# Optimization experiments

Hardware: AMD Instinct MI355X
Metric: run time of the kernel (lower is better)

## Reference

```python
import jax, jax.numpy as jnp
import numpy as np

N, E, H, D = 100000, 800000, 4, 32
IN_DIM, OUT_DIM = 128, 128
NEG_SLOPE = 0.2


def setup_inputs() -> dict:
    key = jax.random.key(0)
    ks = jax.random.split(key, 10)
    x = jax.random.normal(ks[0], (N, IN_DIM), dtype=jnp.float32)
    edge_index = jax.random.randint(ks[1], (2, E), 0, N, dtype=jnp.int32)
    edge_type = jax.random.randint(ks[2], (E,), 0, 3, dtype=jnp.int32)
    s = 0.05  # xavier-ish small init scale
    Wq = jax.random.normal(ks[3], (IN_DIM, H * D), dtype=jnp.float32) * s
    Wk = jax.random.normal(ks[4], (IN_DIM, H * D), dtype=jnp.float32) * s
    Wv = jax.random.normal(ks[5], (IN_DIM, H * D), dtype=jnp.float32) * s
    attn_linear = jax.random.normal(ks[6], (1, H, 2 * D), dtype=jnp.float32) * s
    edge_embed_table = jax.random.normal(ks[7], (3, H * D), dtype=jnp.float32) * s
    Wo = jax.random.normal(ks[8], (H * D, OUT_DIM), dtype=jnp.float32) * s
    bo = jnp.zeros((OUT_DIM,), dtype=jnp.float32)
    return {"x": x, "edge_index": edge_index, "edge_type": edge_type,
            "Wq": Wq, "Wk": Wk, "Wv": Wv, "attn_linear": attn_linear,
            "edge_embed_table": edge_embed_table, "Wo": Wo, "bo": bo}


def reference(x, edge_index, edge_type, Wq, Wk, Wv, attn_linear, edge_embed_table, Wo, bo):
    src, dst = edge_index[0], edge_index[1]
    n = x.shape[0]
    q = (x @ Wq).reshape(n, H, D)
    k = (x @ Wk).reshape(n, H, D)
    v = (x @ Wv).reshape(n, H, D)
    attn_l = attn_linear[:, :, :D]   # (1,H,D)
    attn_r = attn_linear[:, :, D:]
    score_src = (q * attn_l).sum(-1)  # (N,H)
    score_dst = (k * attn_r).sum(-1)
    s = score_src[src] + score_dst[dst]            # (E,H)
    s = jnp.where(s >= 0, s, NEG_SLOPE * s)        # leaky_relu
    ee = edge_embed_table[edge_type].reshape(-1, H, D)  # (E,H,D)
    s = s + (q[src] * ee).sum(-1)
    # sparse softmax over edges grouped by dst (detached max, clamped at -100)
    max_s = jnp.full((n, H), -jnp.inf, dtype=s.dtype).at[dst].max(jax.lax.stop_gradient(s))
    max_s = jnp.maximum(max_s, -100.0)
    exp_s = jnp.exp(s - max_s[dst])
    sum_exp = jax.ops.segment_sum(exp_s, dst, num_segments=n)
    a = jnp.minimum(exp_s / (sum_exp[dst] + 1e-6), 1.0)  # (E,H)
    msgs = a[:, :, None] * v[src]                        # (E,H,D)
    out = jax.ops.segment_sum(msgs, dst, num_segments=n) # (N,H,D)
    out = jnp.clip(out, -50.0, 50.0).reshape(n, H * D)
    return out @ Wo + bo
```

## Files before the change

kernel.cpp:

```cpp
#include <hip/hip_runtime.h>
#include <cstdint>

#define HEADS 4
#define DD    32
#define HD    128
#define SCOL  32
#define NEGS  0.2f

typedef __attribute__((ext_vector_type(8))) short bf16x8;
typedef __attribute__((ext_vector_type(4))) float f32x4;

__device__ __forceinline__ float bl(unsigned u) { return __uint_as_float(u << 16); }
__device__ __forceinline__ float bh(unsigned u) { return __uint_as_float(u & 0xffff0000u); }
__device__ __forceinline__ unsigned short f2b(float f) {
    unsigned u = __float_as_uint(f);
    u += 0x7fffu + ((u >> 16) & 1u);
    return (unsigned short)(u >> 16);
}

__global__ void k_buildC(const float* __restrict__ Wq, const float* __restrict__ Wk,
                         const float* __restrict__ attn, const float* __restrict__ ee,
                         float* __restrict__ C) {
    int tid = blockIdx.x*blockDim.x + threadIdx.x;
    if (tid >= HD*SCOL) return;
    int i = tid >> 5, c = tid & 31;
    float s = 0.f;
    if (c < 8) {
        int h = c & 3;
        const float* w = ((c < 4) ? Wq : Wk) + i*HD + h*DD;
        const float* a = attn + h*64 + ((c < 4) ? 0 : DD);
        #pragma unroll
        for (int d = 0; d < DD; ++d) s += w[d]*a[d];
    } else if (c < 20) {
        int idx = c - 8; int ty = idx >> 2; int h = idx & 3;
        const float* w  = Wq + i*HD + h*DD;
        const float* em = ee + ty*HD + h*DD;
        #pragma unroll
        for (int d = 0; d < DD; ++d) s += w[d]*em[d];
    }
    C[i*SCOL + c] = s;
}

__global__ void k_pack(const float* __restrict__ Wv, const float* __restrict__ C,
                       const float* __restrict__ Wo,
                       unsigned short* __restrict__ Bpv, unsigned short* __restrict__ Bpo) {
    int id = blockIdx.x*256 + threadIdx.x;
    if (id < 20480) {
        int j = id & 7, l = (id >> 3) & 63, tk = id >> 9;
        int t = tk >> 2, kk = tk & 3;
        int k = kk*32 + (l >> 4)*8 + j;
        int n = t*16 + (l & 15);
        float val = (n < HD) ? Wv[k*HD + n] : C[k*SCOL + (n - HD)];
        Bpv[id] = f2b(val);
    } else if (id < 36864) {
        int o = id - 20480;
        int j = o & 7, l = (o >> 3) & 63, tk = o >> 9;
        int t = tk >> 2, kk = tk & 3;
        int k = kk*32 + (l >> 4)*8 + j;
        int n = t*16 + (l & 15);
        Bpo[o] = f2b(Wo[k*HD + n]);
    }
}

__global__ __launch_bounds__(256)
void k_vproj(const float* __restrict__ x, const unsigned short* __restrict__ Bpv,
             unsigned short* __restrict__ vbf, float* __restrict__ scores, int N) {
    __shared__ unsigned short xs[64*136];
    const int t = threadIdx.x;
    const int nbase = blockIdx.x * 64;
    const float4* xg = (const float4*)x;
    #pragma unroll
    for (int k = 0; k < 8; ++k) {
        int fi = t + k*256;
        int row = fi >> 5, c4 = fi & 31;
        int node = nbase + row;
        float4 val = make_float4(0.f,0.f,0.f,0.f);
        if (node < N) val = xg[(size_t)nbase*32 + fi];
        unsigned short p[4] = { f2b(val.x), f2b(val.y), f2b(val.z), f2b(val.w) };
        *(uint2*)((char*)xs + row*272 + c4*8) = *(const uint2*)p;
    }
    __syncthreads();
    const int wid = t >> 6, l = t & 63;
    const int lr = l & 15, lg = l >> 4;
    bf16x8 a[4];
    #pragma unroll
    for (int kk = 0; kk < 4; ++kk)
        a[kk] = *(const bf16x8*)((const char*)xs + (16*wid + lr)*272 + kk*64 + lg*16);
    const bf16x8* Bp = (const bf16x8*)Bpv;
    #pragma unroll
    for (int ct = 0; ct < 10; ++ct) {
        f32x4 acc = {0.f, 0.f, 0.f, 0.f};
        #pragma unroll
        for (int kk = 0; kk < 4; ++kk)
            acc = __builtin_amdgcn_mfma_f32_16x16x32_bf16(a[kk], Bp[(ct*4 + kk)*64 + l], acc, 0, 0, 0);
        if (ct < 8) {
            int col = ct*16 + lr;
            #pragma unroll
            for (int r = 0; r < 4; ++r) {
                int node = nbase + 16*wid + lg*4 + r;
                if (node < N) vbf[(size_t)node*HD + col] = f2b(acc[r]);
            }
        } else {
            int col = (ct - 8)*16 + lr;
            #pragma unroll
            for (int r = 0; r < 4; ++r) {
                int node = nbase + 16*wid + lg*4 + r;
                if (node < N) scores[(size_t)node*SCOL + col] = acc[r];
            }
        }
    }
}

__global__ void k_count(const int* __restrict__ ei, int* __restrict__ counts, int E) {
    int e = blockIdx.x*256 + threadIdx.x;
    if (e < E) atomicAdd(&counts[ei[E + e]], 1);
}

__global__ __launch_bounds__(256)
void k_scan1(const int* __restrict__ counts, int* __restrict__ off,
             int* __restrict__ bsum, int N) {
    __shared__ int sh[256];
    int t = threadIdx.x;
    int base = blockIdx.x*2048 + t*8;
    int vals[8]; int s = 0;
    #pragma unroll
    for (int k = 0; k < 8; ++k) {
        int idx = base + k;
        int cv = (idx < N) ? counts[idx] : 0;
        s += cv; vals[k] = s;
    }
    sh[t] = s;
    __syncthreads();
    for (int o = 1; o < 256; o <<= 1) {
        int v2 = (t >= o) ? sh[t-o] : 0;
        __syncthreads();
        sh[t] += v2;
        __syncthreads();
    }
    int excl = (t > 0) ? sh[t-1] : 0;
    #pragma unroll
    for (int k = 0; k < 8; ++k) {
        int idx = base + k;
        if (idx < N) off[idx+1] = excl + vals[k];
    }
    if (t == 255) bsum[blockIdx.x] = sh[255];
    if (blockIdx.x == 0 && t == 0) off[0] = 0;
}
__global__ void k_scan2(int* __restrict__ bsum, int nb) {
    __shared__ int sh[256];
    int t = threadIdx.x;
    sh[t] = (t < nb) ? bsum[t] : 0;
    __syncthreads();
    for (int o = 1; o < 256; o <<= 1) {
        int v2 = (t >= o) ? sh[t-o] : 0;
        __syncthreads();
        sh[t] += v2;
        __syncthreads();
    }
    if (t < nb) bsum[t] = (t > 0) ? sh[t-1] : 0;
}
__global__ void k_scan3(int* __restrict__ off, const int* __restrict__ bsum, int N) {
    int i = blockIdx.x*256 + threadIdx.x;
    if (i < N) off[i+1] += bsum[i >> 11];
}

__global__ void k_fill(const int* __restrict__ ei, const int* __restrict__ et,
                       const float* __restrict__ scores, int* __restrict__ off,
                       int* __restrict__ ssrc, float4* __restrict__ sw4, int E) {
    int e = blockIdx.x*256 + threadIdx.x;
    if (e >= E) return;
    int src = ei[e], dst = ei[E + e], ty = et[e];
    const float* ps = scores + (size_t)src*SCOL;
    const float* pd = scores + (size_t)dst*SCOL;
    float4 a = *(const float4*)(ps);
    float4 b = *(const float4*)(pd + 4);
    float4 q = *(const float4*)(ps + 8 + 4*ty);
    float4 w;
    float t0;
    t0 = a.x + b.x; w.x = __expf(((t0 >= 0.f) ? t0 : NEGS*t0) + q.x);
    t0 = a.y + b.y; w.y = __expf(((t0 >= 0.f) ? t0 : NEGS*t0) + q.y);
    t0 = a.z + b.z; w.z = __expf(((t0 >= 0.f) ? t0 : NEGS*t0) + q.z);
    t0 = a.w + b.w; w.w = __expf(((t0 >= 0.f) ? t0 : NEGS*t0) + q.w);
    int slot = atomicAdd(&off[dst], 1);
    ssrc[slot] = src;
    sw4[slot]  = w;
}

__global__ __launch_bounds__(256)
void k_agg(const int* __restrict__ off, const int* __restrict__ ssrc,
           const float4* __restrict__ sw4, const unsigned short* __restrict__ vbf,
           unsigned short* __restrict__ outbf, int N) {
    const int wid  = threadIdx.x >> 6;
    const int lane = threadIdx.x & 63;
    const int n = blockIdx.x*4 + wid;
    if (n >= N) return;
    const int start = (n > 0) ? off[n-1] : 0;
    const int end   = off[n];
    const int g  = lane >> 4;
    const int dl = lane & 15;
    const int hh = dl >> 2;
    const float* wf = (const float*)sw4;
    float z = 0.f;
    float c0=0.f,c1=0.f,c2=0.f,c3=0.f,c4=0.f,c5=0.f,c6=0.f,c7=0.f;
    int  sl0 = start + g, sl1 = sl0 + 4;
    bool p0 = sl0 < end, p1 = sl1 < end;
    float w0 = 0.f, w1 = 0.f;
    uint4 v0 = make_uint4(0,0,0,0), v1 = make_uint4(0,0,0,0);
    if (p0) { int s = ssrc[sl0]; w0 = wf[(size_t)sl0*4 + hh];
              v0 = *(const uint4*)&vbf[(size_t)s*HD + dl*8]; }
    if (p1) { int s = ssrc[sl1]; w1 = wf[(size_t)sl1*4 + hh];
              v1 = *(const uint4*)&vbf[(size_t)s*HD + dl*8]; }
    while (p0) {
        int  sl2 = sl0 + 8;
        bool p2 = sl2 < end;
        float w2 = 0.f; uint4 v2 = make_uint4(0,0,0,0);
        if (p2) { int s = ssrc[sl2]; w2 = wf[(size_t)sl2*4 + hh];
                  v2 = *(const uint4*)&vbf[(size_t)s*HD + dl*8]; }
        z  += w0;
        c0 += w0*bl(v0.x); c1 += w0*bh(v0.x);
        c2 += w0*bl(v0.y); c3 += w0*bh(v0.y);
        c4 += w0*bl(v0.z); c5 += w0*bh(v0.z);
        c6 += w0*bl(v0.w); c7 += w0*bh(v0.w);
        sl0 = sl1; p0 = p1; w0 = w1; v0 = v1;
        sl1 = sl2; p1 = p2; w1 = w2; v1 = v2;
    }
    #pragma unroll
    for (int o = 16; o <= 32; o <<= 1) {
        z  += __shfl_xor(z, o);
        c0 += __shfl_xor(c0, o); c1 += __shfl_xor(c1, o);
        c2 += __shfl_xor(c2, o); c3 += __shfl_xor(c3, o);
        c4 += __shfl_xor(c4, o); c5 += __shfl_xor(c5, o);
        c6 += __shfl_xor(c6, o); c7 += __shfl_xor(c7, o);
    }
    if (g == 0) {
        float r = 1.f/(z + 1e-6f);
        unsigned short p[8] = { f2b(c0*r), f2b(c1*r), f2b(c2*r), f2b(c3*r),
                                f2b(c4*r), f2b(c5*r), f2b(c6*r), f2b(c7*r) };
        *(uint4*)&outbf[(size_t)n*HD + dl*8] = *(const uint4*)p;
    }
}

__global__ __launch_bounds__(256)
void k_out(const unsigned short* __restrict__ accbf, const unsigned short* __restrict__ Bpo,
           const float* __restrict__ bo, float* __restrict__ out, int N) {
    const int t = threadIdx.x;
    const int wid = t >> 6, l = t & 63;
    const int tile = blockIdx.x*4 + wid;
    if (tile*16 >= N) return;
    const int lr = l & 15, lg = l >> 4;
    const int r0 = tile*16;
    bf16x8 a[4];
    #pragma unroll
    for (int kk = 0; kk < 4; ++kk)
        a[kk] = *(const bf16x8*)&accbf[(size_t)(r0 + lr)*HD + kk*32 + lg*8];
    const bf16x8* Bp = (const bf16x8*)Bpo;
    #pragma unroll
    for (int ct = 0; ct < 8; ++ct) {
        f32x4 acc = {0.f, 0.f, 0.f, 0.f};
        #pragma unroll
        for (int kk = 0; kk < 4; ++kk)
            acc = __builtin_amdgcn_mfma_f32_16x16x32_bf16(a[kk], Bp[(ct*4 + kk)*64 + l], acc, 0, 0, 0);
        int col = ct*16 + lr;
        float bias = bo[col];
        #pragma unroll
        for (int r = 0; r < 4; ++r) {
            int node = r0 + lg*4 + r;
            if (node < N) out[(size_t)node*HD + col] = acc[r] + bias;
        }
    }
}

extern "C" void kernel_launch(void* const* d_in, const int* in_sizes, int n_in,
                              void* d_out, int out_size, void* d_ws, size_t ws_size,
                              hipStream_t stream) {
    const float* x    = (const float*)d_in[0];
    const int*   ei   = (const int*)  d_in[1];
    const int*   et   = (const int*)  d_in[2];
    const float* Wq   = (const float*)d_in[3];
    const float* Wk   = (const float*)d_in[4];
    const float* Wv   = (const float*)d_in[5];
    const float* attn = (const float*)d_in[6];
    const float* ee   = (const float*)d_in[7];
    const float* Wo   = (const float*)d_in[8];
    const float* bo   = (const float*)d_in[9];
    float* out = (float*)d_out;
    const int N = in_sizes[0] / HD;
    const int E = in_sizes[2];

    char* w = (char*)d_ws;
    auto alloc = [&](size_t bytes) -> void* {
        void* p = (void*)w;
        w += (bytes + 255) & ~(size_t)255;
        return p;
    };
    float*          C      = (float*)         alloc((size_t)HD*SCOL*sizeof(float));
    unsigned short* Bpv    = (unsigned short*)alloc((size_t)20480*sizeof(unsigned short));
    unsigned short* Bpo    = (unsigned short*)alloc((size_t)16384*sizeof(unsigned short));
    unsigned short* vbf    = (unsigned short*)alloc((size_t)N*HD*sizeof(unsigned short));
    float*          scores = (float*)         alloc((size_t)N*SCOL*sizeof(float));
    int*            counts = (int*)           alloc((size_t)N*sizeof(int));
    int*            off    = (int*)           alloc((size_t)(N+1)*sizeof(int));
    int*            bsum   = (int*)           alloc(4096);
    int*            ssrc   = (int*)           alloc((size_t)E*sizeof(int));
    float4*         sw4    = (float4*)        alloc((size_t)E*sizeof(float4));
    unsigned short* outbf  = (unsigned short*)alloc((size_t)N*HD*sizeof(unsigned short));

    hipMemsetAsync(counts, 0, (size_t)N*sizeof(int), stream);
    k_buildC<<<(HD*SCOL + 255)/256, 256, 0, stream>>>(Wq, Wk, attn, ee, C);
    k_pack<<<144, 256, 0, stream>>>(Wv, C, Wo, Bpv, Bpo);
    k_vproj<<<(N + 63)/64, 256, 0, stream>>>(x, Bpv, vbf, scores, N);
    k_count<<<(E + 255)/256, 256, 0, stream>>>(ei, counts, E);
    const int nb = (N + 2047)/2048;
    k_scan1<<<nb, 256, 0, stream>>>(counts, off, bsum, N);
    k_scan2<<<1, 256, 0, stream>>>(bsum, nb);
    k_scan3<<<(N + 255)/256, 256, 0, stream>>>(off, bsum, N);
    k_fill<<<(E + 255)/256, 256, 0, stream>>>(ei, et, scores, off, ssrc, sw4, E);
    k_agg<<<(N + 3)/4, 256, 0, stream>>>(off, ssrc, sw4, vbf, outbf, N);
    k_out<<<(N + 63)/64, 256, 0, stream>>>(outbf, Bpo, bo, out, N);
}
```

Before: 192.2 us.

## Move edge-weight computation into aggregation and pack src/type into one word

The fill kernel no longer computes and stores per-edge float4 exp weights. It only scatters a packed 32-bit (src | type<<20) entry per edge. The aggregation kernel now gathers the source scores and computes the leaky-relu/exp weight itself, which removes the 16-byte weight write and re-read per edge. Each lane now covers 16 features (8 edges in flight per wave instead of 4), so more accumulators are live and register pressure rises. It also adds extra gathers of scores rows and relies on src fitting in 20 bits.

```diff
diff --git a/kernel.cpp b/kernel.cpp
--- a/kernel.cpp
+++ b/kernel.cpp
@@ -164,31 +164,18 @@
     if (i < N) off[i+1] += bsum[i >> 11];
 }
 
-__global__ void k_fill(const int* __restrict__ ei, const int* __restrict__ et,
-                       const float* __restrict__ scores, int* __restrict__ off,
-                       int* __restrict__ ssrc, float4* __restrict__ sw4, int E) {
+__global__ void k_slot(const int* __restrict__ ei, const int* __restrict__ et,
+                       int* __restrict__ off, unsigned* __restrict__ pk, int E) {
     int e = blockIdx.x*256 + threadIdx.x;
     if (e >= E) return;
     int src = ei[e], dst = ei[E + e], ty = et[e];
-    const float* ps = scores + (size_t)src*SCOL;
-    const float* pd = scores + (size_t)dst*SCOL;
-    float4 a = *(const float4*)(ps);
-    float4 b = *(const float4*)(pd + 4);
-    float4 q = *(const float4*)(ps + 8 + 4*ty);
-    float4 w;
-    float t0;
-    t0 = a.x + b.x; w.x = __expf(((t0 >= 0.f) ? t0 : NEGS*t0) + q.x);
-    t0 = a.y + b.y; w.y = __expf(((t0 >= 0.f) ? t0 : NEGS*t0) + q.y);
-    t0 = a.z + b.z; w.z = __expf(((t0 >= 0.f) ? t0 : NEGS*t0) + q.z);
-    t0 = a.w + b.w; w.w = __expf(((t0 >= 0.f) ? t0 : NEGS*t0) + q.w);
     int slot = atomicAdd(&off[dst], 1);
-    ssrc[slot] = src;
-    sw4[slot]  = w;
+    pk[slot] = (unsigned)src | ((unsigned)ty << 20);
 }
 
 __global__ __launch_bounds__(256)
-void k_agg(const int* __restrict__ off, const int* __restrict__ ssrc,
-           const float4* __restrict__ sw4, const unsigned short* __restrict__ vbf,
+void k_agg(const int* __restrict__ off, const unsigned* __restrict__ pk,
+           const float* __restrict__ scores, const unsigned short* __restrict__ vbf,
            unsigned short* __restrict__ outbf, int N) {
     const int wid  = threadIdx.x >> 6;
     const int lane = threadIdx.x & 63;
@@ -196,47 +183,67 @@
     if (n >= N) return;
     const int start = (n > 0) ? off[n-1] : 0;
     const int end   = off[n];
-    const int g  = lane >> 4;
-    const int dl = lane & 15;
-    const int hh = dl >> 2;
-    const float* wf = (const float*)sw4;
+    const int g  = lane >> 3;
+    const int dl = lane & 7;
+    const int hh = dl >> 1;
+    const float sd = scores[(size_t)n*SCOL + 4 + hh];
     float z = 0.f;
-    float c0=0.f,c1=0.f,c2=0.f,c3=0.f,c4=0.f,c5=0.f,c6=0.f,c7=0.f;
-    int  sl0 = start + g, sl1 = sl0 + 4;
-    bool p0 = sl0 < end, p1 = sl1 < end;
-    float w0 = 0.f, w1 = 0.f;
-    uint4 v0 = make_uint4(0,0,0,0), v1 = make_uint4(0,0,0,0);
-    if (p0) { int s = ssrc[sl0]; w0 = wf[(size_t)sl0*4 + hh];
-              v0 = *(const uint4*)&vbf[(size_t)s*HD + dl*8]; }
-    if (p1) { int s = ssrc[sl1]; w1 = wf[(size_t)sl1*4 + hh];
-              v1 = *(const uint4*)&vbf[(size_t)s*HD + dl*8]; }
+    float c[16];
+    #pragma unroll
+    for (int i = 0; i < 16; ++i) c[i] = 0.f;
+
+    int  sl0 = start + g;
+    bool p0 = sl0 < end;
+    float f0 = 0.f, q0 = 0.f;
+    uint4 va0 = make_uint4(0,0,0,0), vb0 = make_uint4(0,0,0,0);
+    if (p0) {
+        unsigned pe = pk[sl0];
+        int s = pe & 0xFFFFF, ty = pe >> 20;
+        const float* ps = scores + (size_t)s*SCOL;
+        f0 = ps[hh]; q0 = ps[8 + 4*ty + hh];
+        const unsigned short* pv = vbf + (size_t)s*HD + dl*16;
+        va0 = *(const uint4*)pv; vb0 = *(const uint4*)(pv + 8);
+    }
     while (p0) {
-        int  sl2 = sl0 + 8;
-        bool p2 = sl2 < end;
-        float w2 = 0.f; uint4 v2 = make_uint4(0,0,0,0);
-        if (p2) { int s = ssrc[sl2]; w2 = wf[(size_t)sl2*4 + hh];
-                  v2 = *(const uint4*)&vbf[(size_t)s*HD + dl*8]; }
-        z  += w0;
-        c0 += w0*bl(v0.x); c1 += w0*bh(v0.x);
-        c2 += w0*bl(v0.y); c3 += w0*bh(v0.y);
-        c4 += w0*bl(v0.z); c5 += w0*bh(v0.z);
-        c6 += w0*bl(v0.w); c7 += w0*bh(v0.w);
-        sl0 = sl1; p0 = p1; w0 = w1; v0 = v1;
-        sl1 = sl2; p1 = p2; w1 = w2; v1 = v2;
-    }
-    #pragma unroll
-    for (int o = 16; o <= 32; o <<= 1) {
-        z  += __shfl_xor(z, o);
-        c0 += __shfl_xor(c0, o); c1 += __shfl_xor(c1, o);
-        c2 += __shfl_xor(c2, o); c3 += __shfl_xor(c3, o);
-        c4 += __shfl_xor(c4, o); c5 += __shfl_xor(c5, o);
-        c6 += __shfl_xor(c6, o); c7 += __shfl_xor(c7, o);
+        int  sl1 = sl0 + 8;
+        bool p1 = sl1 < end;
+        float f1 = 0.f, q1 = 0.f;
+        uint4 va1 = make_uint4(0,0,0,0), vb1 = make_uint4(0,0,0,0);
+        if (p1) {
+            unsigned pe = pk[sl1];
+            int s = pe & 0xFFFFF, ty = pe >> 20;
+            const float* ps = scores + (size_t)s*SCOL;
+            f1 = ps[hh]; q1 = ps[8 + 4*ty + hh];
+            const unsigned short* pv = vbf + (size_t)s*HD + dl*16;
+            va1 = *(const uint4*)pv; vb1 = *(const uint4*)(pv + 8);
+        }
+        float t = f0 + sd;
+        float w = __expf(((t >= 0.f) ? t : NEGS*t) + q0);
+        z += w;
+        c[0] += w*bl(va0.x); c[1] += w*bh(va0.x);
+        c[2] += w*bl(va0.y); c[3] += w*bh(va0.y);
+        c[4] += w*bl(va0.z); c[5] += w*bh(va0.z);
+        c[6] += w*bl(va0.w); c[7] += w*bh(va0.w);
+        c[8] += w*bl(vb0.x); c[9] += w*bh(vb0.x);
+        c[10]+= w*bl(vb0.y); c[11]+= w*bh(vb0.y);
+        c[12]+= w*bl(vb0.z); c[13]+= w*bh(vb0.z);
+        c[14]+= w*bl(vb0.w); c[15]+= w*bh(vb0.w);
+        sl0 = sl1; p0 = p1; f0 = f1; q0 = q1; va0 = va1; vb0 = vb1;
+    }
+    #pragma unroll
+    for (int o = 8; o <= 32; o <<= 1) {
+        z += __shfl_xor(z, o);
+        #pragma unroll
+        for (int i = 0; i < 16; ++i) c[i] += __shfl_xor(c[i], o);
     }
     if (g == 0) {
         float r = 1.f/(z + 1e-6f);
-        unsigned short p[8] = { f2b(c0*r), f2b(c1*r), f2b(c2*r), f2b(c3*r),
-                                f2b(c4*r), f2b(c5*r), f2b(c6*r), f2b(c7*r) };
-        *(uint4*)&outbf[(size_t)n*HD + dl*8] = *(const uint4*)p;
+        unsigned short pbuf[16];
+        #pragma unroll
+        for (int i = 0; i < 16; ++i) pbuf[i] = f2b(c[i]*r);
+        unsigned short* po = outbf + (size_t)n*HD + dl*16;
+        *(uint4*)po       = *(const uint4*)pbuf;
+        *(uint4*)(po + 8) = *(const uint4*)(pbuf + 8);
     }
 }
 
@@ -301,8 +308,7 @@
     int*            counts = (int*)           alloc((size_t)N*sizeof(int));
     int*            off    = (int*)           alloc((size_t)(N+1)*sizeof(int));
     int*            bsum   = (int*)           alloc(4096);
-    int*            ssrc   = (int*)           alloc((size_t)E*sizeof(int));
-    float4*         sw4    = (float4*)        alloc((size_t)E*sizeof(float4));
+    unsigned*       pk     = (unsigned*)      alloc((size_t)E*sizeof(unsigned));
     unsigned short* outbf  = (unsigned short*)alloc((size_t)N*HD*sizeof(unsigned short));
 
     hipMemsetAsync(counts, 0, (size_t)N*sizeof(int), stream);
@@ -314,7 +320,7 @@
     k_scan1<<<nb, 256, 0, stream>>>(counts, off, bsum, N);
     k_scan2<<<1, 256, 0, stream>>>(bsum, nb);
     k_scan3<<<(N + 255)/256, 256, 0, stream>>>(off, bsum, N);
-    k_fill<<<(E + 255)/256, 256, 0, stream>>>(ei, et, scores, off, ssrc, sw4, E);
-    k_agg<<<(N + 3)/4, 256, 0, stream>>>(off, ssrc, sw4, vbf, outbf, N);
+    k_slot<<<(E + 255)/256, 256, 0, stream>>>(ei, et, off, pk, E);
+    k_agg<<<(N + 3)/4, 256, 0, stream>>>(off, pk, scores, vbf, outbf, N);
     k_out<<<(N + 63)/64, 256, 0, stream>>>(outbf, Bpo, bo, out, N);
 }
```

New measurement: 204.7 us. 6.5% more time.
